# Performance work log

Measured on AMD Instinct MI355X. Metric: run time of the kernel, lower is better.

Reference implementation:

```python
import jax, jax.numpy as jnp
import numpy as np

E = 1024

def setup_inputs() -> dict:
    key = jax.random.key(0)
    ks = jax.random.split(key, 9)
    s = 1.0 / np.sqrt(E)
    return {
        "x": jax.random.normal(ks[0], (4, 2048, E), dtype=jnp.float32),
        "Wq": jax.random.uniform(ks[1], (E, E), jnp.float32, -s, s),
        "bq": jax.random.uniform(ks[2], (E,), jnp.float32, -s, s),
        "Wk": jax.random.uniform(ks[3], (E, E), jnp.float32, -s, s),
        "bk": jax.random.uniform(ks[4], (E,), jnp.float32, -s, s),
        "Wv": jax.random.uniform(ks[5], (E, E), jnp.float32, -s, s),
        "bv": jax.random.uniform(ks[6], (E,), jnp.float32, -s, s),
        "Wo": jax.random.uniform(ks[7], (E, E), jnp.float32, -s, s),
        "bo": jax.random.uniform(ks[8], (E,), jnp.float32, -s, s),
    }

def reference(x, Wq, bq, Wk, bk, Wv, bv, Wo, bo):
    # Note: the torch module never splits heads; attention is over full embed_dim.
    # nn.Linear: y = x @ W.T + b
    Q = jnp.einsum('bse,fe->bsf', x, Wq) + bq
    K = jnp.einsum('bse,fe->bsf', x, Wk) + bk
    V = jnp.einsum('bse,fe->bsf', x, Wv) + bv
    scale = 1.0 / jnp.sqrt(jnp.asarray(x.shape[-1], x.dtype))
    scores = jnp.einsum('bqe,bke->bqk', Q, K) * scale  # [B, S, S]
    weights = jax.nn.softmax(scores, axis=-1)
    out = jnp.einsum('bqk,bke->bqe', weights, V)
    # dropout is identity in eval mode
    return jnp.einsum('bse,fe->bsf', out, Wo) + bo
```

## Files before the change

kernel.cpp:

```cpp
#include <hip/hip_runtime.h>
#include <hip/hip_bf16.h>
#include <stdint.h>

typedef short bf16x8 __attribute__((ext_vector_type(8)));
typedef float f32x4 __attribute__((ext_vector_type(4)));
typedef __attribute__((address_space(3))) void lds_void_t;
typedef __attribute__((address_space(1))) void g_void_t;

static __device__ __forceinline__ unsigned short f2b(float f) {
    __hip_bfloat16 b = __float2bfloat16(f);
    return __builtin_bit_cast(unsigned short, b);
}
static __device__ __forceinline__ float b2f(unsigned int u) {
    return __builtin_bit_cast(float, u << 16);
}

__global__ __launch_bounds__(256) void prep(
    const float* __restrict__ x,
    const float* __restrict__ wq, const float* __restrict__ wk,
    const float* __restrict__ wv, const float* __restrict__ wo,
    const float* __restrict__ bq, const float* __restrict__ bk,
    const float* __restrict__ bv_, float* __restrict__ bqkv,
    ushort* __restrict__ xb, ushort* __restrict__ wqkvb)
{
    const int T = 3145728;
    int i = blockIdx.x * 256 + threadIdx.x;
    const int stride = gridDim.x * 256;
    for (; i < T; i += stride) {
        const float* src; ushort* dst; int off;
        if (i < 2097152) { src = x; dst = xb; off = i; }
        else {
            const int j = i - 2097152;
            const int w = j >> 18;
            off = j & 262143;
            src = (w == 0) ? wq : (w == 1) ? wk : (w == 2) ? wv : wo;
            dst = wqkvb + (w << 20);
        }
        float4 v = reinterpret_cast<const float4*>(src)[off];
        ushort4 o;
        o.x = f2b(v.x); o.y = f2b(v.y); o.z = f2b(v.z); o.w = f2b(v.w);
        reinterpret_cast<ushort4*>(dst)[off] = o;
    }
    const int t = blockIdx.x * 256 + threadIdx.x;
    if (t < 3072) {
        const int sec = t >> 10, of = t & 1023;
        bqkv[t] = sec == 0 ? bq[of] : (sec == 1 ? bk[of] : bv_[of]);
    }
}

template<typename CT, bool HAS_BIAS>
__global__ __launch_bounds__(256, 4)
void gemm_bt(const ushort* __restrict__ A, const ushort* __restrict__ B,
             const float* __restrict__ bias, CT* __restrict__ C,
             int lda, int ldb, int ldc, int K,
             long strideA, long strideB, long strideC, float alpha)
{
    __shared__ __align__(16) ushort smem[128 * 64 * 2];
    ushort* sA = smem;
    ushort* sB = smem + 128 * 64;

    const int bz = blockIdx.z;
    A += (size_t)bz * strideA;
    B += (size_t)bz * strideB;
    C += (size_t)bz * strideC;

    const int gx = gridDim.x, gy = gridDim.y;
    const int nwg = gx * gy;
    int bx = blockIdx.x, by = blockIdx.y;
    if ((nwg & 7) == 0) {
        const int flat = blockIdx.x + gx * blockIdx.y;
        const int cpx = nwg >> 3;
        const int u = (flat & 7) * cpx + (flat >> 3);
        bx = u % gx;
        by = u / gx;
    }

    const int tid = threadIdx.x;
    const int w   = tid >> 6;
    const int l   = tid & 63;
    const int wr  = w >> 1;
    const int wc  = w & 1;

    const int bRow = by * 128;
    const int bCol = bx * 128;

    const int lr   = l >> 3;
    const int scol = (((l & 7) ^ lr) << 3);

    f32x4 acc[4][4];
#pragma unroll
    for (int m = 0; m < 4; ++m)
#pragma unroll
        for (int n = 0; n < 4; ++n)
            acc[m][n] = f32x4{0.f, 0.f, 0.f, 0.f};

    for (int k0 = 0; k0 < K; k0 += 64) {
#pragma unroll
        for (int p = 0; p < 4; ++p) {
            const int c   = p * 4 + w;
            const int row = c * 8 + lr;
            const ushort* gA = A + (size_t)(bRow + row) * lda + (k0 + scol);
            const ushort* gB = B + (size_t)(bCol + row) * ldb + (k0 + scol);
            __builtin_amdgcn_global_load_lds((const g_void_t*)gA,
                (lds_void_t*)((char*)sA + c * 1024), 16, 0, 0);
            __builtin_amdgcn_global_load_lds((const g_void_t*)gB,
                (lds_void_t*)((char*)sB + c * 1024), 16, 0, 0);
        }
        __syncthreads();

        bf16x8 af[4][2], bfv[4][2];
#pragma unroll
        for (int m = 0; m < 4; ++m) {
            const int ar = wr * 64 + m * 16 + (l & 15);
#pragma unroll
            for (int ks = 0; ks < 2; ++ks) {
                const int slot = (ks * 4 + (l >> 4)) ^ (ar & 7);
                af[m][ks] = *reinterpret_cast<const bf16x8*>(
                    (const char*)sA + ar * 128 + slot * 16);
            }
        }
#pragma unroll
        for (int n = 0; n < 4; ++n) {
            const int br = wc * 64 + n * 16 + (l & 15);
#pragma unroll
            for (int ks = 0; ks < 2; ++ks) {
                const int slot = (ks * 4 + (l >> 4)) ^ (br & 7);
                bfv[n][ks] = *reinterpret_cast<const bf16x8*>(
                    (const char*)sB + br * 128 + slot * 16);
            }
        }
#pragma unroll
        for (int ks = 0; ks < 2; ++ks)
#pragma unroll
            for (int m = 0; m < 4; ++m)
#pragma unroll
                for (int n = 0; n < 4; ++n)
                    acc[m][n] = __builtin_amdgcn_mfma_f32_16x16x32_bf16(
                        af[m][ks], bfv[n][ks], acc[m][n], 0, 0, 0);
        __syncthreads();
    }

    const int cl = l & 15;
    if constexpr (sizeof(CT) == 2) {
        ushort* st = smem;
#pragma unroll
        for (int n = 0; n < 4; ++n) {
            const int col = wc * 64 + n * 16 + cl;
            const float bv = HAS_BIAS ? bias[bCol + col] : 0.f;
#pragma unroll
            for (int m = 0; m < 4; ++m) {
                const int row0 = wr * 64 + m * 16 + (l >> 4) * 4;
#pragma unroll
                for (int r = 0; r < 4; ++r)
                    st[(row0 + r) * 128 + col] = f2b((acc[m][n][r] + bv) * alpha);
            }
        }
        __syncthreads();
#pragma unroll
        for (int i = 0; i < 8; ++i) {
            const int c    = tid + i * 256;
            const int row  = c >> 4;
            const int col8 = (c & 15) * 8;
            *reinterpret_cast<uint4*>(
                (ushort*)C + (size_t)(bRow + row) * ldc + bCol + col8) =
                *reinterpret_cast<const uint4*>(st + row * 128 + col8);
        }
    } else {
#pragma unroll
        for (int n = 0; n < 4; ++n) {
            const int col = bCol + wc * 64 + n * 16 + cl;
            const float bv = HAS_BIAS ? bias[col] : 0.f;
#pragma unroll
            for (int m = 0; m < 4; ++m) {
#pragma unroll
                for (int r = 0; r < 4; ++r) {
                    const int row = bRow + wr * 64 + m * 16 + (l >> 4) * 4 + r;
                    ((float*)C)[(size_t)row * ldc + col] = (acc[m][n][r] + bv) * alpha;
                }
            }
        }
    }
}

__global__ __launch_bounds__(256) void softmax_rows(ushort* __restrict__ S)
{
    __shared__ float red[8];
    const size_t row = blockIdx.x;
    ushort* p = S + row * 2048;
    const int tid = threadIdx.x;

    uint4 v = reinterpret_cast<uint4*>(p)[tid];
    float f[8];
    const unsigned int* wv = reinterpret_cast<const unsigned int*>(&v);
#pragma unroll
    for (int j = 0; j < 4; ++j) {
        f[2 * j]     = b2f(wv[j] & 0xFFFFu);
        f[2 * j + 1] = b2f(wv[j] >> 16);
    }
    float mx = f[0];
#pragma unroll
    for (int j = 1; j < 8; ++j) mx = fmaxf(mx, f[j]);
#pragma unroll
    for (int s = 1; s < 64; s <<= 1) mx = fmaxf(mx, __shfl_xor(mx, s));
    if ((tid & 63) == 0) red[tid >> 6] = mx;
    __syncthreads();
    mx = fmaxf(fmaxf(red[0], red[1]), fmaxf(red[2], red[3]));

    float sum = 0.f;
#pragma unroll
    for (int j = 0; j < 8; ++j) { f[j] = __expf(f[j] - mx); sum += f[j]; }
#pragma unroll
    for (int s = 1; s < 64; s <<= 1) sum += __shfl_xor(sum, s);
    if ((tid & 63) == 0) red[4 + (tid >> 6)] = sum;
    __syncthreads();
    sum = (red[4] + red[5]) + (red[6] + red[7]);
    const float inv = 1.0f / sum;

    uint4 o;
    unsigned int* wo = reinterpret_cast<unsigned int*>(&o);
#pragma unroll
    for (int j = 0; j < 4; ++j) {
        const unsigned int lo = f2b(f[2 * j] * inv);
        const unsigned int hi = f2b(f[2 * j + 1] * inv);
        wo[j] = lo | (hi << 16);
    }
    reinterpret_cast<uint4*>(p)[tid] = o;
}

__global__ __launch_bounds__(256) void transpose_v(
    const ushort* __restrict__ V, ushort* __restrict__ Vt, int ldv, long strideV)
{
    __shared__ ushort t[64][65];
    const int b  = blockIdx.z;
    const int e0 = blockIdx.x * 64;
    const int s0 = blockIdx.y * 64;
    const int tid = threadIdx.x;
    const int cg = (tid & 15) * 4;
    const int r0 = tid >> 4;

    const ushort* Vb = V + (size_t)b * strideV;
#pragma unroll
    for (int p = 0; p < 4; ++p) {
        const int r = r0 + p * 16;
        ushort4 x = *reinterpret_cast<const ushort4*>(
            Vb + (size_t)(s0 + r) * ldv + e0 + cg);
        t[r][cg + 0] = x.x; t[r][cg + 1] = x.y;
        t[r][cg + 2] = x.z; t[r][cg + 3] = x.w;
    }
    __syncthreads();
    ushort* Vtb = Vt + (size_t)b * 1024 * 2048;
#pragma unroll
    for (int p = 0; p < 4; ++p) {
        const int e = r0 + p * 16;
        ushort4 o;
        o.x = t[cg + 0][e]; o.y = t[cg + 1][e];
        o.z = t[cg + 2][e]; o.w = t[cg + 3][e];
        *reinterpret_cast<ushort4*>(Vtb + (size_t)(e0 + e) * 2048 + s0 + cg) = o;
    }
}

extern "C" void kernel_launch(void* const* d_in, const int* in_sizes, int n_in,
                              void* d_out, int out_size, void* d_ws, size_t ws_size,
                              hipStream_t stream)
{
    const float* x  = (const float*)d_in[0];
    const float* Wq = (const float*)d_in[1];
    const float* bq = (const float*)d_in[2];
    const float* Wk = (const float*)d_in[3];
    const float* bk = (const float*)d_in[4];
    const float* Wv = (const float*)d_in[5];
    const float* bv = (const float*)d_in[6];
    const float* Wo = (const float*)d_in[7];
    const float* bo = (const float*)d_in[8];

    char* ws = (char*)d_ws;
    ushort* xb    = (ushort*)(ws);
    ushort* Wqkvb = (ushort*)(ws + 16777216);
    ushort* Wob   = Wqkvb + 3 * 1048576;
    float*  bqkv  = (float*) (ws + 25165824);
    ushort* QKVb  = (ushort*)(ws + 26214400);
    ushort* Vtb   = (ushort*)(ws + 76546048);
    ushort* Sb    = (ushort*)(ws + 93323264);
    ushort* Ob    = (ushort*)(ws + 126877696);

    prep<<<2048, 256, 0, stream>>>(x, Wq, Wk, Wv, Wo, bq, bk, bv, bqkv, xb, Wqkvb);

    gemm_bt<ushort, true><<<dim3(24, 64, 1), 256, 0, stream>>>(
        xb, Wqkvb, bqkv, QKVb, 1024, 1024, 3072, 1024, 0, 0, 0, 1.0f);

    transpose_v<<<dim3(16, 32, 4), 256, 0, stream>>>(
        QKVb + 2048, Vtb, 3072, 2048L * 3072);

    gemm_bt<ushort, false><<<dim3(16, 16, 4), 256, 0, stream>>>(
        QKVb, QKVb + 1024, nullptr, Sb, 3072, 3072, 2048, 1024,
        2048L * 3072, 2048L * 3072, 2048L * 2048, 0.03125f);

    softmax_rows<<<8192, 256, 0, stream>>>(Sb);

    gemm_bt<ushort, false><<<dim3(8, 16, 4), 256, 0, stream>>>(
        Sb, Vtb, nullptr, Ob, 2048, 2048, 1024, 2048,
        2048L * 2048, 1024L * 2048, 2048L * 1024, 1.0f);

    gemm_bt<float, true><<<dim3(8, 64, 1), 256, 0, stream>>>(
        Ob, Wob, bo, (float*)d_out, 1024, 1024, 1024, 1024, 0, 0, 0, 1.0f);
}
```

Measured before the change: 293.6 us.

## Add 256x256 double-buffered GEMM kernel for QKV projection and score GEMMs

```diff
diff --git a/kernel.cpp b/kernel.cpp
--- a/kernel.cpp
+++ b/kernel.cpp
@@ -48,16 +48,14 @@
     }
 }
 
-template<typename CT, bool HAS_BIAS>
-__global__ __launch_bounds__(256, 4)
-void gemm_bt(const ushort* __restrict__ A, const ushort* __restrict__ B,
-             const float* __restrict__ bias, CT* __restrict__ C,
-             int lda, int ldb, int ldc, int K,
-             long strideA, long strideB, long strideC, float alpha)
-{
-    __shared__ __align__(16) ushort smem[128 * 64 * 2];
-    ushort* sA = smem;
-    ushort* sB = smem + 128 * 64;
+template<bool HAS_BIAS>
+__global__ __launch_bounds__(512, 2)
+void gemm256_bt(const ushort* __restrict__ A, const ushort* __restrict__ B,
+                const float* __restrict__ bias, ushort* __restrict__ C,
+                int lda, int ldb, int ldc, int K,
+                long strideA, long strideB, long strideC, float alpha)
+{
+    __shared__ __align__(16) ushort smem[2][2][16384];
 
     const int bz = blockIdx.z;
     A += (size_t)bz * strideA;
@@ -78,6 +76,162 @@
     const int tid = threadIdx.x;
     const int w   = tid >> 6;
     const int l   = tid & 63;
+    const int wr  = w >> 2;
+    const int wc  = w & 3;
+
+    const int bRow = by * 256;
+    const int bCol = bx * 256;
+
+    const int lr   = l >> 3;
+    const int scol = (((l & 7) ^ lr) << 3);
+
+    f32x4 acc[8][4];
+#pragma unroll
+    for (int m = 0; m < 8; ++m)
+#pragma unroll
+        for (int n = 0; n < 4; ++n)
+            acc[m][n] = f32x4{0.f, 0.f, 0.f, 0.f};
+
+    const int NT = K >> 6;
+
+#pragma unroll
+    for (int p = 0; p < 4; ++p) {
+        const int c = w * 4 + p;
+        const ushort* gA = A + (size_t)(bRow + c * 8 + lr) * lda + scol;
+        const ushort* gB = B + (size_t)(bCol + c * 8 + lr) * ldb + scol;
+        __builtin_amdgcn_global_load_lds((const g_void_t*)gA,
+            (lds_void_t*)((char*)&smem[0][0][0] + c * 1024), 16, 0, 0);
+        __builtin_amdgcn_global_load_lds((const g_void_t*)gB,
+            (lds_void_t*)((char*)&smem[0][1][0] + c * 1024), 16, 0, 0);
+    }
+    __syncthreads();
+
+    int cur = 0;
+    bf16x8 af[4][2], bfr[2][2];
+    for (int t = 0; t < NT; ++t) {
+        const char* sAc = (const char*)&smem[cur][0][0];
+        const char* sBc = (const char*)&smem[cur][1][0];
+        char* sAn = (char*)&smem[cur ^ 1][0][0];
+        char* sBn = (char*)&smem[cur ^ 1][1][0];
+        const int k1  = (t + 1) << 6;
+        const bool pre = (t + 1 < NT);
+
+#pragma unroll
+        for (int p = 0; p < 4; ++p) {
+            const int mh = p >> 1;
+            const int nh = (p == 1 || p == 2) ? 1 : 0;
+            if (p == 0 || p == 2) {
+#pragma unroll
+                for (int i = 0; i < 4; ++i) {
+                    const int ar = wr * 128 + (mh * 4 + i) * 16 + (l & 15);
+#pragma unroll
+                    for (int ks = 0; ks < 2; ++ks) {
+                        const int slot = (ks * 4 + (l >> 4)) ^ (ar & 7);
+                        af[i][ks] = *reinterpret_cast<const bf16x8*>(
+                            sAc + ar * 128 + slot * 16);
+                    }
+                }
+            }
+            if (p != 2) {
+#pragma unroll
+                for (int j = 0; j < 2; ++j) {
+                    const int br = wc * 64 + (nh * 2 + j) * 16 + (l & 15);
+#pragma unroll
+                    for (int ks = 0; ks < 2; ++ks) {
+                        const int slot = (ks * 4 + (l >> 4)) ^ (br & 7);
+                        bfr[j][ks] = *reinterpret_cast<const bf16x8*>(
+                            sBc + br * 128 + slot * 16);
+                    }
+                }
+            }
+            if (pre) {
+                const int c = w * 4 + p;
+                const ushort* gA = A + (size_t)(bRow + c * 8 + lr) * lda + (k1 + scol);
+                const ushort* gB = B + (size_t)(bCol + c * 8 + lr) * ldb + (k1 + scol);
+                __builtin_amdgcn_global_load_lds((const g_void_t*)gA,
+                    (lds_void_t*)(sAn + c * 1024), 16, 0, 0);
+                __builtin_amdgcn_global_load_lds((const g_void_t*)gB,
+                    (lds_void_t*)(sBn + c * 1024), 16, 0, 0);
+            }
+            __builtin_amdgcn_s_setprio(1);
+#pragma unroll
+            for (int ks = 0; ks < 2; ++ks)
+#pragma unroll
+                for (int i = 0; i < 4; ++i)
+#pragma unroll
+                    for (int j = 0; j < 2; ++j)
+                        acc[mh * 4 + i][nh * 2 + j] =
+                            __builtin_amdgcn_mfma_f32_16x16x32_bf16(
+                                af[i][ks], bfr[j][ks],
+                                acc[mh * 4 + i][nh * 2 + j], 0, 0, 0);
+            __builtin_amdgcn_s_setprio(0);
+            __builtin_amdgcn_sched_barrier(0);
+        }
+        __syncthreads();
+        cur ^= 1;
+    }
+
+    ushort* st = (ushort*)smem;
+    const int cl = l & 15;
+#pragma unroll
+    for (int n = 0; n < 4; ++n) {
+        const int col = wc * 64 + n * 16 + cl;
+        const float bv = HAS_BIAS ? bias[bCol + col] : 0.f;
+#pragma unroll
+        for (int m = 0; m < 8; ++m) {
+            const int row0 = wr * 128 + m * 16 + (l >> 4) * 4;
+#pragma unroll
+            for (int r = 0; r < 4; ++r) {
+                const int row = row0 + r;
+                const int sl  = ((col >> 3) ^ (row & 7));
+                st[row * 256 + (sl << 3) + (col & 7)] =
+                    f2b((acc[m][n][r] + bv) * alpha);
+            }
+        }
+    }
+    __syncthreads();
+#pragma unroll
+    for (int i = 0; i < 16; ++i) {
+        const int c    = tid + (i << 9);
+        const int row  = c >> 5;
+        const int slot = (c & 31) ^ (row & 7);
+        const uint4 v = *reinterpret_cast<const uint4*>(
+            (const char*)st + row * 512 + slot * 16);
+        *reinterpret_cast<uint4*>(
+            C + (size_t)(bRow + row) * ldc + bCol + ((c & 31) << 3)) = v;
+    }
+}
+
+template<typename CT, bool HAS_BIAS>
+__global__ __launch_bounds__(256, 4)
+void gemm_bt(const ushort* __restrict__ A, const ushort* __restrict__ B,
+             const float* __restrict__ bias, CT* __restrict__ C,
+             int lda, int ldb, int ldc, int K,
+             long strideA, long strideB, long strideC, float alpha)
+{
+    __shared__ __align__(16) ushort smem[128 * 64 * 2];
+    ushort* sA = smem;
+    ushort* sB = smem + 128 * 64;
+
+    const int bz = blockIdx.z;
+    A += (size_t)bz * strideA;
+    B += (size_t)bz * strideB;
+    C += (size_t)bz * strideC;
+
+    const int gx = gridDim.x, gy = gridDim.y;
+    const int nwg = gx * gy;
+    int bx = blockIdx.x, by = blockIdx.y;
+    if ((nwg & 7) == 0) {
+        const int flat = blockIdx.x + gx * blockIdx.y;
+        const int cpx = nwg >> 3;
+        const int u = (flat & 7) * cpx + (flat >> 3);
+        bx = u % gx;
+        by = u / gx;
+    }
+
+    const int tid = threadIdx.x;
+    const int w   = tid >> 6;
+    const int l   = tid & 63;
     const int wr  = w >> 1;
     const int wc  = w & 1;
 
@@ -285,13 +439,13 @@
 
     prep<<<2048, 256, 0, stream>>>(x, Wq, Wk, Wv, Wo, bq, bk, bv, bqkv, xb, Wqkvb);
 
-    gemm_bt<ushort, true><<<dim3(24, 64, 1), 256, 0, stream>>>(
+    gemm256_bt<true><<<dim3(12, 32, 1), 512, 0, stream>>>(
         xb, Wqkvb, bqkv, QKVb, 1024, 1024, 3072, 1024, 0, 0, 0, 1.0f);
 
     transpose_v<<<dim3(16, 32, 4), 256, 0, stream>>>(
         QKVb + 2048, Vtb, 3072, 2048L * 3072);
 
-    gemm_bt<ushort, false><<<dim3(16, 16, 4), 256, 0, stream>>>(
+    gemm256_bt<false><<<dim3(8, 8, 4), 512, 0, stream>>>(
         QKVb, QKVb + 1024, nullptr, Sb, 3072, 3072, 2048, 1024,
         2048L * 3072, 2048L * 3072, 2048L * 2048, 0.03125f);
 
```

New measurement: 294.5 us. No clear change (+0.3%).
